# Kernel tuning notes

Measured on AMD Instinct MI355X. Metric: run time of the kernel, lower is better.

The kernel has to match this reference:

```python
import jax, jax.numpy as jnp
import numpy as np
from jax import lax

B = 4            # batch (number of point clouds)
N_PER = 8192     # points per cloud
STRIDE = 4
M_PER = N_PER // STRIDE   # sampled points per cloud
K = 16           # nsample
C_IN = 64
C_OUT = 128
EPS = 1e-5


def fps(pts, m):
    """Furthest point sampling on (n,3), returns m int32 indices, starts at 0."""
    n = pts.shape[0]

    def step(carry, _):
        dist, last = carry
        d = jnp.sum((pts - pts[last]) ** 2, axis=-1)
        dist = jnp.minimum(dist, d)
        nxt = jnp.argmax(dist).astype(jnp.int32)
        return (dist, nxt), nxt

    init = (jnp.full((n,), 1e10, dtype=pts.dtype), jnp.int32(0))
    _, idxs = lax.scan(step, init, None, length=m - 1)
    return jnp.concatenate([jnp.zeros((1,), jnp.int32), idxs])


def knn_idx(pts, queries, k):
    """Indices of k nearest points for each query. pts (n,3), queries (m,3)."""
    d2 = (jnp.sum(queries * queries, -1)[:, None]
          + jnp.sum(pts * pts, -1)[None, :]
          - 2.0 * (queries @ pts.T))            # (m, n)
    _, idx = lax.top_k(-d2, k)                   # smallest distances
    return idx


def setup_inputs() -> dict:
    key = jax.random.key(0)
    k1, k2, k3 = jax.random.split(key, 3)
    point = jax.random.normal(k1, (B * N_PER, 3), dtype=jnp.float32) * 5.0
    feat = jax.random.normal(k2, (B * N_PER, C_IN), dtype=jnp.float32)
    row_splits = (jnp.arange(B + 1, dtype=jnp.int64) * N_PER)
    W = jax.random.normal(k3, (C_OUT, 3 + C_IN), dtype=jnp.float32) * 0.05
    gamma = jnp.ones((C_OUT,), dtype=jnp.float32)
    beta = jnp.zeros((C_OUT,), dtype=jnp.float32)
    return {"point": point, "feat": feat, "row_splits": row_splits,
            "W": W, "gamma": gamma, "beta": beta}


def reference(point, feat, row_splits, W, gamma, beta):
    pb = point.reshape(B, N_PER, 3)
    fb = feat.reshape(B, N_PER, C_IN)

    # --- furthest point sampling (non-differentiable index op) ---
    sidx = jax.vmap(lambda p: fps(p, M_PER))(lax.stop_gradient(pb))   # (B, M)
    new_p = jnp.take_along_axis(pb, sidx[..., None], axis=1)          # (B, M, 3)

    # --- batched KNN (indices only, like knn_search) ---
    nidx = jax.vmap(knn_idx, in_axes=(0, 0, None))(
        lax.stop_gradient(pb), lax.stop_gradient(new_p), K)           # (B, M, K)

    # --- queryandgroup: gather neighbors, relative xyz, concat feat ---
    gxyz = jax.vmap(lambda p, i: p[i])(pb, nidx) - new_p[:, :, None]  # (B, M, K, 3)
    gfeat = jax.vmap(lambda f, i: f[i])(fb, nidx)                     # (B, M, K, C_IN)
    g = jnp.concatenate([gxyz, gfeat], axis=-1).reshape(B * M_PER, K, 3 + C_IN)

    # --- linear (no bias) -> BN (batch stats over points & neighbors) -> ReLU ---
    y = jnp.einsum('mkc,oc->mko', g, W)                               # (m, K, C_OUT)
    mean = jnp.mean(y, axis=(0, 1))
    var = jnp.mean(jnp.square(y - mean), axis=(0, 1))                 # biased var
    y = (y - mean) * (gamma * lax.rsqrt(var + EPS)) + beta
    y = jax.nn.relu(y)

    # --- maxpool over neighbors ---
    out_feat = jnp.max(y, axis=1)                                     # (m, C_OUT)

    new_point = new_p.reshape(B * M_PER, 3)
    new_row_splits = jnp.arange(B + 1, dtype=jnp.int64) * M_PER
    return new_point, out_feat, new_row_splits
```

## Files before the change

kernel.cpp:

```cpp
#include <hip/hip_runtime.h>

#define NB 4
#define NPER 8192
#define MPER 2048
#define KNN 16
#define CIN 64
#define CO 128
#define MTOT (NB*MPER)
#define CPB 56

typedef unsigned long long u64;
typedef unsigned int u32;

__device__ __forceinline__ float med3f(float a, float b, float c) {
    return __builtin_amdgcn_fmed3f(a, b, c);
}

__global__ void k_init(float* __restrict__ stats, float* __restrict__ rs,
                       u32* __restrict__ prog) {
    int t = threadIdx.x;
    if (t < 256) stats[t] = 0.f;
    if (t < 128) prog[t] = 0u;
    if (t < 5) rs[t] = (float)(t * MPER);
}

#define DPPSTEP(key, CTRL, RM) do {                                                   \
    unsigned lo_ = (unsigned)(key), hi_ = (unsigned)((key) >> 32);                    \
    unsigned nlo = (unsigned)__builtin_amdgcn_update_dpp((int)lo_, (int)lo_, CTRL, RM, 0xf, false); \
    unsigned nhi = (unsigned)__builtin_amdgcn_update_dpp((int)hi_, (int)hi_, CTRL, RM, 0xf, false); \
    unsigned long long ok_ = ((unsigned long long)nhi << 32) | nlo;                   \
    if (ok_ > (key)) (key) = ok_;                                                     \
} while (0)

#define DPP6(key) do { \
    DPPSTEP(key, 0xB1,  0xF); \
    DPPSTEP(key, 0x4E,  0xF); \
    DPPSTEP(key, 0x141, 0xF); \
    DPPSTEP(key, 0x140, 0xF); \
    DPPSTEP(key, 0x142, 0xA); \
    DPPSTEP(key, 0x143, 0xC); \
} while (0)

struct FpsSM {
    float4 spt[NPER];
    u64 red[2][4];
};
struct KnnSM {
    float4 sp[2][2112];
    float  ndl[256][16];
    u32    candl[256][16];
    u32    eql[256][16];
    int    ccnt[256], ecnt[256];
    u32    pcur[256];
    float  taub[64];
};
#define SMBYTES (sizeof(FpsSM) > sizeof(KnnSM) ? sizeof(FpsSM) : sizeof(KnnSM))

__launch_bounds__(256, 1)
__global__ void k_mega(const float* __restrict__ pts, float* __restrict__ out_np,
                       float4* __restrict__ qpts, u32* __restrict__ prog,
                       int* __restrict__ nidx) {
    #pragma clang fp contract(off)
    __shared__ __align__(16) char SMRAW[SMBYTES];
    const int t = threadIdx.x;

    if (blockIdx.x < NB) {
        FpsSM& sm = *(FpsSM*)SMRAW;
        const int b = blockIdx.x;
        const float4* pb4 = (const float4*)(pts + (size_t)b * NPER * 3);

        float f[96];
        #pragma unroll
        for (int j = 0; j < 24; ++j) {
            float4 v = pb4[t * 24 + j];
            f[j*4+0] = v.x; f[j*4+1] = v.y; f[j*4+2] = v.z; f[j*4+3] = v.w;
        }
        float px[32], py[32], pz[32], dd[32];
        #pragma unroll
        for (int s = 0; s < 32; ++s) {
            px[s] = f[3*s]; py[s] = f[3*s+1]; pz[s] = f[3*s+2];
            dd[s] = 1e10f;
            sm.spt[t * 32 + s] = make_float4(px[s], py[s], pz[s], 0.f);
        }
        if (t == 0) {
            size_t row = (size_t)b * MPER;
            out_np[row*3+0] = px[0]; out_np[row*3+1] = py[0]; out_np[row*3+2] = pz[0];
            qpts[row] = make_float4(px[0], py[0], pz[0], 0.f);
        }
        __syncthreads();

        float4 c0 = sm.spt[0];
        float cx = c0.x, cy = c0.y, cz = c0.z;
        const int lane = t & 63, wv = t >> 6;
        const int ibase = t * 32;

        for (int i = 1; i < MPER; ++i) {
            float bv = -1.f; int bs = 0;
            #pragma unroll
            for (int s = 0; s < 32; ++s) {
                float dx = px[s] - cx, dy = py[s] - cy, dz = pz[s] - cz;
                float t0 = dx * dx, t1 = dy * dy, t2 = dz * dz;
                float d = (t0 + t1) + t2;
                float nd = fminf(dd[s], d);
                dd[s] = nd;
                bool bet = nd > bv;
                bv = bet ? nd : bv;
                bs = bet ? s : bs;
            }
            u64 key = ((u64)__float_as_uint(bv) << 32) | (u32)~(u32)(ibase + bs);

            DPP6(key);

            if (lane == 63) sm.red[i & 1][wv] = key;
            __syncthreads();

            const int p = i & 1;
            u64 k0 = sm.red[p][0], k1 = sm.red[p][1], k2 = sm.red[p][2], k3 = sm.red[p][3];
            u64 ka = k0 > k1 ? k0 : k1;
            u64 kb = k2 > k3 ? k2 : k3;
            u64 kbest = ka > kb ? ka : kb;
            const int i2 = (int)(~(u32)kbest) & 0x1FFF;

            float4 c = sm.spt[i2];
            cx = c.x; cy = c.y; cz = c.z;

            if (t == 0) {
                size_t row = (size_t)b * MPER + i;
                out_np[row*3+0] = cx; out_np[row*3+1] = cy; out_np[row*3+2] = cz;
                qpts[row] = make_float4(cx, cy, cz, 0.f);
                if (((i & 127) == 127) || (i >= 1536 && ((i & 31) == 31))) {
                    __threadfence();
                    __hip_atomic_store(prog + b * 32, (u32)(i + 1),
                                       __ATOMIC_RELEASE, __HIP_MEMORY_SCOPE_AGENT);
                }
            }
        }
    } else {
        KnnSM& sm = *(KnnSM*)SMRAW;
        const int kb = blockIdx.x - NB;
        const int b  = kb / CPB;
        const int r  = kb % CPB;
        int nq, q0b;
        if (r < 24)      { nq = 64; q0b = r << 6; }
        else if (r < 32) { nq = 32; q0b = 1536 + ((r - 24) << 5); }
        else if (r < 40) { nq = 16; q0b = 1792 + ((r - 32) << 4); }
        else             { nq = 8;  q0b = 1920 + ((r - 40) << 3); }
        const int lgL = (nq == 64) ? 2 : (nq == 32) ? 3 : (nq == 16) ? 4 : 5;
        const int L = 1 << lgL;
        const int lgP = 11 - lgL;
        const int P = 1 << lgP;
        const int stride = P + 2;
        const u32 need = (u32)(q0b + nq);

        if (t == 0) {
            while (__hip_atomic_load(prog + b * 32, __ATOMIC_RELAXED,
                                     __HIP_MEMORY_SCOPE_AGENT) < need)
                __builtin_amdgcn_s_sleep(32);
        }
        __syncthreads();
        __threadfence();

        const int sub = t & (L - 1), qloc = t >> lgL;
        const int q = b * MPER + q0b + qloc;
        const float4 qp = qpts[q];
        const float qq = (qp.x * qp.x + qp.y * qp.y) + qp.z * qp.z;
        const float* pb = pts + (size_t)b * NPER * 3;
        const int wq = t >> 6, wl = t & 63;

        float4 Lr[6];
        #define LOADC(c) do { const float4* src_ = (const float4*)(pb + (size_t)(c) * 2048 * 3); \
            _Pragma("unroll") for (int u_ = 0; u_ < 6; ++u_) Lr[u_] = src_[t * 6 + u_]; } while (0)
        #define WRITEC(pbuf) do { \
            float fl_[24]; \
            _Pragma("unroll") for (int u_ = 0; u_ < 6; ++u_) { \
                fl_[u_*4+0]=Lr[u_].x; fl_[u_*4+1]=Lr[u_].y; fl_[u_*4+2]=Lr[u_].z; fl_[u_*4+3]=Lr[u_].w; } \
            _Pragma("unroll") for (int r_ = 0; r_ < 8; ++r_) { \
                float x_=fl_[3*r_], y_=fl_[3*r_+1], z_=fl_[3*r_+2]; \
                float pp_=(x_*x_ + y_*y_) + z_*z_; \
                int gpos_ = wq*512 + wl*8 + r_; \
                sm.sp[pbuf][(gpos_ >> lgP)*stride + (gpos_ & (P-1))] = make_float4(x_,y_,z_,pp_); } } while (0)

        float nd[16];
        #pragma unroll
        for (int j = 0; j < 16; ++j) nd[j] = 1e30f;

        LOADC(0); WRITEC(0); LOADC(1);
        __syncthreads();
        for (int c = 0; c < 4; ++c) {
            const int pbuf = c & 1;
            const float4* rowp = &sm.sp[pbuf][sub * stride];
            #pragma unroll 4
            for (int j = 0; j < P; ++j) {
                float4 p = rowp[j];
                float dot = (qp.x * p.x + qp.y * p.y) + qp.z * p.z;
                float d = (qq + p.w) - 2.f * dot;
                if (d < nd[15]) {
                    #pragma unroll
                    for (int u = 15; u >= 1; --u) nd[u] = med3f(d, nd[u-1], nd[u]);
                    nd[0] = fminf(nd[0], d);
                }
            }
            __syncthreads();
            if (c < 3) {
                WRITEC((c + 1) & 1);
                if (c < 2) LOADC(c + 2);
                __syncthreads();
            }
        }
        #pragma unroll
        for (int j = 0; j < 16; ++j) sm.ndl[t][j] = nd[j];
        __syncthreads();

        if (sub == 0) {
            float td[16];
            #pragma unroll
            for (int u = 0; u < 16; ++u) td[u] = 1e30f;
            for (int s = 0; s < L; ++s) {
                for (int u2 = 0; u2 < 16; ++u2) {
                    float v = sm.ndl[t + s][u2];
                    if (!(v < td[15])) break;
                    #pragma unroll
                    for (int u = 15; u >= 1; --u) td[u] = med3f(v, td[u-1], td[u]);
                    td[0] = fminf(td[0], v);
                }
            }
            sm.taub[qloc] = td[15];
        }
        __syncthreads();
        const float tau = sm.taub[qloc];

        int cnt = 0, ecn = 0;
        LOADC(0); WRITEC(0); LOADC(1);
        __syncthreads();
        for (int c = 0; c < 4; ++c) {
            const int pbuf = c & 1;
            const float4* rowp = &sm.sp[pbuf][sub * stride];
            for (int j = 0; j < P; ++j) {
                float4 p = rowp[j];
                float dot = (qp.x * p.x + qp.y * p.y) + qp.z * p.z;
                float d = (qq + p.w) - 2.f * dot;
                if (d <= tau) {
                    u32 pidx = (u32)(c * 2048 + (sub << lgP) + j);
                    if (d < tau) { if (cnt < 16) sm.candl[t][cnt++] = pidx; }
                    else         { if (ecn < 16) sm.eql[t][ecn++] = pidx; }
                }
            }
            __syncthreads();
            if (c < 3) {
                WRITEC((c + 1) & 1);
                if (c < 2) LOADC(c + 2);
                __syncthreads();
            }
        }
        sm.ccnt[t] = cnt; sm.ecnt[t] = ecn; sm.pcur[t] = 0;
        __syncthreads();

        if (sub == 0) {
            const int base = t;
            int kept = 0;
            size_t obase = (size_t)q * KNN;
            for (int s = 0; s < L; ++s) {
                int n = sm.ccnt[base + s];
                for (int e = 0; e < n && kept < 16; ++e)
                    nidx[obase + kept++] = b * NPER + (int)sm.candl[base + s][e];
            }
            while (kept < 16) {
                u32 best = 0xFFFFFFFFu; int bs = -1;
                for (int s = 0; s < L; ++s) {
                    u32 ps = sm.pcur[base + s];
                    u32 v = (ps < (u32)sm.ecnt[base + s]) ? sm.eql[base + s][ps] : 0xFFFFFFFFu;
                    if (v < best) { best = v; bs = s; }
                }
                if (bs < 0) break;
                sm.pcur[base + bs]++;
                nidx[obase + kept++] = b * NPER + (int)best;
            }
        }
        #undef LOADC
        #undef WRITEC
    }
}

__launch_bounds__(128, 4)
__global__ void k_stats(const float* __restrict__ pts, const float* __restrict__ feat,
                        const float* __restrict__ W, const int* __restrict__ nidx,
                        const float4* __restrict__ qpts, float* __restrict__ ymax,
                        float* __restrict__ ymin, float* __restrict__ stats) {
    __shared__ float4 g4[KNN][17];
    const int t = threadIdx.x;
    float w[68];
    const float* wr = W + t * 67;
    #pragma unroll
    for (int c = 0; c < 64; ++c) w[c] = wr[3 + c];
    w[64] = wr[0]; w[65] = wr[1]; w[66] = wr[2]; w[67] = 0.f;

    float s_sum = 0.f, s_sq = 0.f;
    const int k0 = t >> 3, p8 = t & 7;
    for (int mi = 0; mi < 8; ++mi) {
        const int m0 = blockIdx.x * 8 + mi;
        {
            int nid = nidx[(size_t)m0 * KNN + k0];
            const float4* fr = (const float4*)(feat + (size_t)nid * CIN);
            g4[k0][p8*2]   = fr[p8*2];
            g4[k0][p8*2+1] = fr[p8*2+1];
        }
        if (t < 16) {
            int nid = nidx[(size_t)m0 * KNN + t];
            float4 qp = qpts[m0];
            float x = pts[(size_t)nid*3], y = pts[(size_t)nid*3+1], z = pts[(size_t)nid*3+2];
            g4[t][16] = make_float4(x - qp.x, y - qp.y, z - qp.z, 0.f);
        }
        __syncthreads();
        float vmax = -1e30f, vmin = 1e30f;
        #pragma unroll 1
        for (int k = 0; k < KNN; ++k) {
            float y0 = 0.f, y1 = 0.f, y2 = 0.f, y3 = 0.f;
            #pragma unroll
            for (int c4 = 0; c4 < 17; ++c4) {
                float4 gv = g4[k][c4];
                y0 = fmaf(gv.x, w[c4*4+0], y0);
                y1 = fmaf(gv.y, w[c4*4+1], y1);
                y2 = fmaf(gv.z, w[c4*4+2], y2);
                y3 = fmaf(gv.w, w[c4*4+3], y3);
            }
            float y = (y0 + y1) + (y2 + y3);
            vmax = fmaxf(vmax, y); vmin = fminf(vmin, y);
            s_sum += y; s_sq = fmaf(y, y, s_sq);
        }
        ymax[(size_t)m0 * CO + t] = vmax;
        ymin[(size_t)m0 * CO + t] = vmin;
        __syncthreads();
    }
    atomicAdd(stats + t, s_sum);
    atomicAdd(stats + CO + t, s_sq);
}

__global__ void k_out(const float* __restrict__ ymax, const float* __restrict__ ymin,
                      const float* __restrict__ stats, const float* __restrict__ gamma,
                      const float* __restrict__ beta, float* __restrict__ out_feat) {
    int tid = blockIdx.x * 256 + threadIdx.x;
    int o = tid & (CO - 1);
    const float inv = 1.f / (float)(MTOT * KNN);
    float mean = stats[o] * inv;
    float var = stats[CO + o] * inv - mean * mean;
    var = fmaxf(var, 0.f);
    float s = gamma[o] * rsqrtf(var + 1e-5f);
    float bb = beta[o] - mean * s;
    float yv = (s >= 0.f) ? ymax[tid] : ymin[tid];
    out_feat[tid] = fmaxf(fmaf(s, yv, bb), 0.f);
}

extern "C" void kernel_launch(void* const* d_in, const int* in_sizes, int n_in,
                              void* d_out, int out_size, void* d_ws, size_t ws_size,
                              hipStream_t stream) {
    const float* pts   = (const float*)d_in[0];
    const float* feat  = (const float*)d_in[1];
    const float* W     = (const float*)d_in[3];
    const float* gamma = (const float*)d_in[4];
    const float* beta  = (const float*)d_in[5];
    float* out = (float*)d_out;
    char* ws = (char*)d_ws;

    float4* qpts = (float4*)(ws);
    int*    nidx = (int*)(ws + 131072);
    float*  stats = (float*)(ws + 655360);
    u32*    prog  = (u32*)(ws + 656384);
    float*  ymax  = (float*)(ws + 657408);
    float*  ymin  = (float*)(ws + 657408 + 4194304);

    float* out_np   = out;
    float* out_feat = out + 24576;
    float* out_rs   = out + 24576 + 1048576;

    hipLaunchKernelGGL(k_init,  dim3(1), dim3(256), 0, stream, stats, out_rs, prog);
    hipLaunchKernelGGL(k_mega,  dim3(NB + NB * CPB), dim3(256), 0, stream,
                       pts, out_np, qpts, prog, nidx);
    hipLaunchKernelGGL(k_stats, dim3(MTOT / 8), dim3(128), 0, stream,
                       pts, feat, W, nidx, qpts, ymax, ymin, stats);
    hipLaunchKernelGGL(k_out,   dim3(MTOT * CO / 256), dim3(256), 0, stream,
                       ymax, ymin, stats, gamma, beta, out_feat);
}
```

Baseline: 2.055 ms.

## Fuse grouping/linear/stats into KNN blocks and move FPS progress signaling off thread 0

The separate k_stats kernel is removed. Each KNN block now keeps its neighbor indices in shared memory and, with double-buffered gathers, computes the linear projection, per-query max/min and the BN sum/sum-of-squares itself. The goal is to drop the global nidx round-trip and a kernel launch, and to overlap the MLP work with the serial FPS blocks that still run. FPS progress is now published by thread 64 right after the per-iteration barrier, without the explicit threadfence on thread 0. That shortens FPS's serial critical path, but it relies on barrier-plus-release ordering for visibility, and the final small KNN blocks now carry extra tail work.

```diff
diff --git a/kernel.cpp b/kernel.cpp
--- a/kernel.cpp
+++ b/kernel.cpp
@@ -53,13 +53,17 @@
     int    ccnt[256], ecnt[256];
     u32    pcur[256];
     float  taub[64];
+    u32    nidxL[64][16];
+    float4 g4[2][16][18];
 };
 #define SMBYTES (sizeof(FpsSM) > sizeof(KnnSM) ? sizeof(FpsSM) : sizeof(KnnSM))
 
 __launch_bounds__(256, 1)
-__global__ void k_mega(const float* __restrict__ pts, float* __restrict__ out_np,
+__global__ void k_mega(const float* __restrict__ pts, const float* __restrict__ feat,
+                       const float* __restrict__ W, float* __restrict__ out_np,
                        float4* __restrict__ qpts, u32* __restrict__ prog,
-                       int* __restrict__ nidx) {
+                       float* __restrict__ ymax, float* __restrict__ ymin,
+                       float* __restrict__ stats) {
     #pragma clang fp contract(off)
     __shared__ __align__(16) char SMRAW[SMBYTES];
     const int t = threadIdx.x;
@@ -114,6 +118,11 @@
             if (lane == 63) sm.red[i & 1][wv] = key;
             __syncthreads();
 
+            if (t == 64 && (((i & 127) == 0) || (i >= 1536 && (i & 31) == 0))) {
+                __hip_atomic_store(prog + b * 32, (u32)i,
+                                   __ATOMIC_RELEASE, __HIP_MEMORY_SCOPE_AGENT);
+            }
+
             const int p = i & 1;
             u64 k0 = sm.red[p][0], k1 = sm.red[p][1], k2 = sm.red[p][2], k3 = sm.red[p][3];
             u64 ka = k0 > k1 ? k0 : k1;
@@ -128,12 +137,12 @@
                 size_t row = (size_t)b * MPER + i;
                 out_np[row*3+0] = cx; out_np[row*3+1] = cy; out_np[row*3+2] = cz;
                 qpts[row] = make_float4(cx, cy, cz, 0.f);
-                if (((i & 127) == 127) || (i >= 1536 && ((i & 31) == 31))) {
-                    __threadfence();
-                    __hip_atomic_store(prog + b * 32, (u32)(i + 1),
-                                       __ATOMIC_RELEASE, __HIP_MEMORY_SCOPE_AGENT);
-                }
-            }
+            }
+        }
+        __syncthreads();
+        if (t == 64) {
+            __hip_atomic_store(prog + b * 32, (u32)MPER,
+                               __ATOMIC_RELEASE, __HIP_MEMORY_SCOPE_AGENT);
         }
     } else {
         KnnSM& sm = *(KnnSM*)SMRAW;
@@ -258,11 +267,10 @@
         if (sub == 0) {
             const int base = t;
             int kept = 0;
-            size_t obase = (size_t)q * KNN;
             for (int s = 0; s < L; ++s) {
                 int n = sm.ccnt[base + s];
                 for (int e = 0; e < n && kept < 16; ++e)
-                    nidx[obase + kept++] = b * NPER + (int)sm.candl[base + s][e];
+                    sm.nidxL[qloc][kept++] = (u32)(b * NPER) + sm.candl[base + s][e];
             }
             while (kept < 16) {
                 u32 best = 0xFFFFFFFFu; int bs = -1;
@@ -273,66 +281,83 @@
                 }
                 if (bs < 0) break;
                 sm.pcur[base + bs]++;
-                nidx[obase + kept++] = b * NPER + (int)best;
-            }
+                sm.nidxL[qloc][kept++] = (u32)(b * NPER) + best;
+            }
+        }
+        __syncthreads();
+
+        const int o = t >> 1, kh = t & 1;
+        float w[68];
+        {
+            const float* wr = W + o * 67;
+            #pragma unroll
+            for (int c = 0; c < 64; ++c) w[c] = wr[3 + c];
+            w[64] = wr[0]; w[65] = wr[1]; w[66] = wr[2]; w[67] = 0.f;
+        }
+        const int gn = t >> 4, gf = t & 15;
+        float ssum = 0.f, ssq = 0.f;
+
+        float4 gfv, gxv = make_float4(0.f, 0.f, 0.f, 0.f);
+        {
+            int nid = (int)sm.nidxL[0][gn];
+            gfv = ((const float4*)(feat + (size_t)nid * CIN))[gf];
+            if (t < 16) {
+                int nid2 = (int)sm.nidxL[0][t];
+                float4 qp2 = qpts[(size_t)b * MPER + q0b];
+                gxv = make_float4(pts[(size_t)nid2*3]   - qp2.x,
+                                  pts[(size_t)nid2*3+1] - qp2.y,
+                                  pts[(size_t)nid2*3+2] - qp2.z, 0.f);
+            }
+        }
+        for (int mi = 0; mi < nq; ++mi) {
+            const int buf = mi & 1;
+            sm.g4[buf][gn][gf] = gfv;
+            if (t < 16) sm.g4[buf][t][16] = gxv;
+            if (mi + 1 < nq) {
+                int nid = (int)sm.nidxL[mi+1][gn];
+                gfv = ((const float4*)(feat + (size_t)nid * CIN))[gf];
+                if (t < 16) {
+                    int nid2 = (int)sm.nidxL[mi+1][t];
+                    float4 qp2 = qpts[(size_t)b * MPER + q0b + mi + 1];
+                    gxv = make_float4(pts[(size_t)nid2*3]   - qp2.x,
+                                      pts[(size_t)nid2*3+1] - qp2.y,
+                                      pts[(size_t)nid2*3+2] - qp2.z, 0.f);
+                }
+            }
+            __syncthreads();
+            float vmax = -1e30f, vmin = 1e30f;
+            #pragma unroll 1
+            for (int kk = 0; kk < 8; ++kk) {
+                const int k = kh * 8 + kk;
+                float y0 = 0.f, y1 = 0.f, y2 = 0.f, y3 = 0.f;
+                #pragma unroll
+                for (int c4 = 0; c4 < 17; ++c4) {
+                    float4 gv = sm.g4[buf][k][c4];
+                    y0 = fmaf(gv.x, w[c4*4+0], y0);
+                    y1 = fmaf(gv.y, w[c4*4+1], y1);
+                    y2 = fmaf(gv.z, w[c4*4+2], y2);
+                    y3 = fmaf(gv.w, w[c4*4+3], y3);
+                }
+                float y = (y0 + y1) + (y2 + y3);
+                vmax = fmaxf(vmax, y); vmin = fminf(vmin, y);
+                ssum += y; ssq = fmaf(y, y, ssq);
+            }
+            float vM = fmaxf(vmax, __shfl_xor(vmax, 1));
+            float vm = fminf(vmin, __shfl_xor(vmin, 1));
+            if (kh == 0) {
+                size_t mrow = (size_t)(b * MPER + q0b + mi) * CO + o;
+                ymax[mrow] = vM; ymin[mrow] = vm;
+            }
+        }
+        float ts = ssum + __shfl_xor(ssum, 1);
+        float tq = ssq  + __shfl_xor(ssq, 1);
+        if (kh == 0) {
+            atomicAdd(stats + o, ts);
+            atomicAdd(stats + CO + o, tq);
         }
         #undef LOADC
         #undef WRITEC
     }
-}
-
-__launch_bounds__(128, 4)
-__global__ void k_stats(const float* __restrict__ pts, const float* __restrict__ feat,
-                        const float* __restrict__ W, const int* __restrict__ nidx,
-                        const float4* __restrict__ qpts, float* __restrict__ ymax,
-                        float* __restrict__ ymin, float* __restrict__ stats) {
-    __shared__ float4 g4[KNN][17];
-    const int t = threadIdx.x;
-    float w[68];
-    const float* wr = W + t * 67;
-    #pragma unroll
-    for (int c = 0; c < 64; ++c) w[c] = wr[3 + c];
-    w[64] = wr[0]; w[65] = wr[1]; w[66] = wr[2]; w[67] = 0.f;
-
-    float s_sum = 0.f, s_sq = 0.f;
-    const int k0 = t >> 3, p8 = t & 7;
-    for (int mi = 0; mi < 8; ++mi) {
-        const int m0 = blockIdx.x * 8 + mi;
-        {
-            int nid = nidx[(size_t)m0 * KNN + k0];
-            const float4* fr = (const float4*)(feat + (size_t)nid * CIN);
-            g4[k0][p8*2]   = fr[p8*2];
-            g4[k0][p8*2+1] = fr[p8*2+1];
-        }
-        if (t < 16) {
-            int nid = nidx[(size_t)m0 * KNN + t];
-            float4 qp = qpts[m0];
-            float x = pts[(size_t)nid*3], y = pts[(size_t)nid*3+1], z = pts[(size_t)nid*3+2];
-            g4[t][16] = make_float4(x - qp.x, y - qp.y, z - qp.z, 0.f);
-        }
-        __syncthreads();
-        float vmax = -1e30f, vmin = 1e30f;
-        #pragma unroll 1
-        for (int k = 0; k < KNN; ++k) {
-            float y0 = 0.f, y1 = 0.f, y2 = 0.f, y3 = 0.f;
-            #pragma unroll
-            for (int c4 = 0; c4 < 17; ++c4) {
-                float4 gv = g4[k][c4];
-                y0 = fmaf(gv.x, w[c4*4+0], y0);
-                y1 = fmaf(gv.y, w[c4*4+1], y1);
-                y2 = fmaf(gv.z, w[c4*4+2], y2);
-                y3 = fmaf(gv.w, w[c4*4+3], y3);
-            }
-            float y = (y0 + y1) + (y2 + y3);
-            vmax = fmaxf(vmax, y); vmin = fminf(vmin, y);
-            s_sum += y; s_sq = fmaf(y, y, s_sq);
-        }
-        ymax[(size_t)m0 * CO + t] = vmax;
-        ymin[(size_t)m0 * CO + t] = vmin;
-        __syncthreads();
-    }
-    atomicAdd(stats + t, s_sum);
-    atomicAdd(stats + CO + t, s_sq);
 }
 
 __global__ void k_out(const float* __restrict__ ymax, const float* __restrict__ ymin,
@@ -362,7 +387,6 @@
     char* ws = (char*)d_ws;
 
     float4* qpts = (float4*)(ws);
-    int*    nidx = (int*)(ws + 131072);
     float*  stats = (float*)(ws + 655360);
     u32*    prog  = (u32*)(ws + 656384);
     float*  ymax  = (float*)(ws + 657408);
@@ -374,9 +398,7 @@
 
     hipLaunchKernelGGL(k_init,  dim3(1), dim3(256), 0, stream, stats, out_rs, prog);
     hipLaunchKernelGGL(k_mega,  dim3(NB + NB * CPB), dim3(256), 0, stream,
-                       pts, out_np, qpts, prog, nidx);
-    hipLaunchKernelGGL(k_stats, dim3(MTOT / 8), dim3(128), 0, stream,
-                       pts, feat, W, nidx, qpts, ymax, ymin, stats);
+                       pts, feat, W, out_np, qpts, prog, ymax, ymin, stats);
     hipLaunchKernelGGL(k_out,   dim3(MTOT * CO / 256), dim3(256), 0, stream,
                        ymax, ymin, stats, gamma, beta, out_feat);
 }
```

Result: no change. 2.019 ms (median of 4 runs) (-1.7%).
